# Kernel tuning notes

Hardware: AMD Instinct MI355X
Metric: run time of the kernel (lower is better)

Reference implementation:

```python
import jax, jax.numpy as jnp
import numpy as np
from jax import lax

BN_EPS = 1e-5


def binarize(v):
    """Sign binarization with clipped straight-through estimator.
    Forward: sign(v). Backward: grad * 1{|v| <= 1} (hardtanh STE), matching
    the standard 1w1a BinaryFunction used in XNOR/IR-Net style repos."""
    clipped = jnp.clip(v, -1.0, 1.0)
    return clipped + lax.stop_gradient(jnp.sign(v) - clipped)


def setup_inputs() -> dict:
    key = jax.random.key(0)
    k1, k2, k3, k4 = jax.random.split(key, 4)
    x = jax.random.normal(k1, (32, 256, 56, 56), dtype=jnp.float32)
    w = jax.random.normal(k2, (256, 256, 3, 3), dtype=jnp.float32) * 0.05
    gamma = jax.random.uniform(k3, (256,), dtype=jnp.float32, minval=0.5, maxval=1.5)
    beta = jax.random.normal(k4, (256,), dtype=jnp.float32) * 0.1
    return {"x": x, "w": w, "gamma": gamma, "beta": beta}


def reference(x, w, gamma, beta):
    # Binarize activations and weights (1-bit each) -> XNOR-style conv in FP math.
    bx = binarize(x)                       # [N, C_in, H, W] in {-1, 0, +1}
    bw = binarize(w)                       # [C_out, C_in, kH, kW]
    y = lax.conv_general_dilated(
        bx, bw,
        window_strides=(1, 1),
        padding=((1, 1), (1, 1)),
        dimension_numbers=("NCHW", "OIHW", "NCHW"),
    )                                      # [N, C_out, H, W]
    # BatchNorm2d in training mode: batch statistics over N, H, W per channel.
    mean = jnp.mean(y, axis=(0, 2, 3))
    var = jnp.var(y, axis=(0, 2, 3))
    inv = lax.rsqrt(var + BN_EPS)
    out = (y - mean[None, :, None, None]) * (gamma * inv)[None, :, None, None] \
        + beta[None, :, None, None]
    return out
```

## Files before the change

kernel.cpp:

```cpp
#include <hip/hip_runtime.h>
#include <stdint.h>

typedef unsigned long long u64;
typedef unsigned int u32;
typedef int v4i  __attribute__((ext_vector_type(4)));
typedef int v16i __attribute__((ext_vector_type(16)));

#define N_IMG 32
#define C_IN  256
#define C_OUT 256
#define H     56
#define W     56
#define HW    (H*W)
#define NHW   (N_IMG*HW)
#define CHW   (C_IN*HW)

#define PX_BYTES  3211264
#define WPK_BYTES 589824
#define Y_OFF     (PX_BYTES + WPK_BYTES)

__global__ __launch_bounds__(256)
void pack_x_kernel(const float* __restrict__ x, u64* __restrict__ px) {
    int t = blockIdx.x * 256 + threadIdx.x;
    int w4   = t % 14;
    int r    = t / 14;
    int word = r & 3;
    int r2   = r >> 2;
    int h    = r2 % H;
    int n    = r2 / H;
    const float4* src = (const float4*)(x + ((size_t)(n*C_IN + word*64) * HW + h*W + w4*4));
    u64 b0 = 0, b1 = 0, b2 = 0, b3 = 0;
    #pragma unroll 8
    for (int j = 0; j < 64; ++j) {
        float4 v = src[(size_t)j * (HW/4)];
        b0 |= (u64)(__float_as_uint(v.x) >> 31) << j;
        b1 |= (u64)(__float_as_uint(v.y) >> 31) << j;
        b2 |= (u64)(__float_as_uint(v.z) >> 31) << j;
        b3 |= (u64)(__float_as_uint(v.w) >> 31) << j;
    }
    u64* dst = px + (((size_t)((n*H + h)*W + w4*4)) << 2) + word;
    dst[0] = b0; dst[4] = b1; dst[8] = b2; dst[12] = b3;
}

__global__ __launch_bounds__(256)
void pack_wpk_kernel(const float* __restrict__ wt, char* __restrict__ wpk) {
    int t = blockIdx.x * 256 + threadIdx.x;
    int co = t & 255;
    int tk = t >> 8;
    int tap = tk >> 3;
    int kb  = tk & 7;
    u32* out = (u32*)wpk + t*8;
    #pragma unroll
    for (int g = 0; g < 8; ++g) {
        u32 dw = 0;
        #pragma unroll
        for (int b = 0; b < 4; ++b) {
            int ci = kb*32 + 4*g + b;
            float v = wt[((size_t)(co*C_IN + ci)) * 9 + tap];
            u32 byte = (__float_as_uint(v) >> 31) ? 0xFFu : 0x01u;
            dw |= byte << (8*b);
        }
        out[g] = dw;
    }
}

__global__ __launch_bounds__(256, 2)
void conv_mfma_kernel(const u64* __restrict__ px, const char* __restrict__ wpk,
                      short* __restrict__ y) {
    __shared__ char lds[4*4*66*16];
    int bx = blockIdx.x;
    int n  = bx / 28;
    int h0 = (bx % 28) * 2;
    int cobase = blockIdx.y * 128;
    int tid = threadIdx.x;

    int wid   = tid >> 6;
    int lane  = tid & 63;
    int l31   = lane & 31;
    int lhalf = lane >> 5;
    int coq   = wid & 1;
    int pxh   = wid >> 1;
    int cot   = cobase + coq*64;

    int pj0 = pxh*64 + l31;
    int pj1 = pj0 + 32;
    int r0 = (pj0 >= 56) ? 1 : 0;
    int w0 = pj0 - 56*r0;
    int r1 = (pj1 >= 56) ? 1 : 0;
    int w1 = pj1 - 56*r1; if (w1 > 55) w1 = 55;

    v16i acc00 = {0,0,0,0,0,0,0,0,0,0,0,0,0,0,0,0};
    v16i acc01 = acc00;
    v16i acc10 = acc00;
    v16i acc11 = acc00;

    const v4i* wq = (const v4i*)wpk;

    #pragma unroll 1
    for (int ciq = 0; ciq < 4; ++ciq) {
        if (ciq) __syncthreads();
        for (int i = tid; i < 4*66; i += 256) {
            int row = i / 66;
            int wp  = i % 66;
            int hh = h0 + row - 1;
            int ww = wp - 1;
            bool valid = ((unsigned)hh < (unsigned)H) && ((unsigned)ww < (unsigned)W);
            u64 wv = 0;
            if (valid)
                wv = px[(((size_t)((n*H + hh)*W + ww)) << 2) + ciq];
            u32 basev = valid ? 0x01010101u : 0u;
            #pragma unroll
            for (int kc = 0; kc < 4; ++kc) {
                u32 bits = (u32)(wv >> (kc*16)) & 0xFFFFu;
                v4i ov;
                #pragma unroll
                for (int d = 0; d < 4; ++d) {
                    u32 sel = (bits >> (4*d)) & 0xFu;
                    u32 sp  = (sel * 0x204081u) & 0x01010101u;
                    u32 m   = (sp << 8) - (sp << 1);
                    ov[d] = (int)(basev + m);
                }
                *(v4i*)(lds + ((kc*264 + i) << 4)) = ov;
            }
        }
        __syncthreads();

        #pragma unroll
        for (int tap = 0; tap < 9; ++tap) {
            const int dw = tap % 3;
            const int rr = tap / 3;
            int i0 = (((r0 + rr)*66) + (w0 + dw)) << 4;
            int i1 = (((r1 + rr)*66) + (w1 + dw)) << 4;
            #pragma unroll
            for (int kb = 0; kb < 2; ++kb) {
                int kbg = ciq*2 + kb;
                int widx = ((tap*8 + kbg)*256 + cot + l31) << 1;
                v4i av0 = wq[widx | lhalf];
                v4i av1 = wq[(widx + 64) | lhalf];
                int kc = kb*2 + lhalf;
                v4i b0 = *(const v4i*)(lds + kc*4224 + i0);
                v4i b1 = *(const v4i*)(lds + kc*4224 + i1);
                acc00 = __builtin_amdgcn_mfma_i32_32x32x32_i8(av0, b0, acc00, 0, 0, 0);
                acc01 = __builtin_amdgcn_mfma_i32_32x32x32_i8(av0, b1, acc01, 0, 0, 0);
                acc10 = __builtin_amdgcn_mfma_i32_32x32x32_i8(av1, b0, acc10, 0, 0, 0);
                acc11 = __builtin_amdgcn_mfma_i32_32x32x32_i8(av1, b1, acc11, 0, 0, 0);
            }
        }
    }

    size_t yb0 = (size_t)n*CHW + (size_t)(cot + (lhalf << 2))*HW;
    size_t yb1 = yb0 + (size_t)32*HW;
    int hr0 = h0 + r0, hr1 = h0 + r1;
    bool full1 = !(pxh == 1 && l31 >= 16);
    {
        size_t o = yb0 + (size_t)hr0*W + w0;
        #pragma unroll
        for (int rg = 0; rg < 16; ++rg)
            y[o + (size_t)((rg&3) + 8*(rg>>2))*HW] = (short)acc00[rg];
    }
    {
        size_t o = yb1 + (size_t)hr0*W + w0;
        #pragma unroll
        for (int rg = 0; rg < 16; ++rg)
            y[o + (size_t)((rg&3) + 8*(rg>>2))*HW] = (short)acc10[rg];
    }
    if (full1) {
        size_t o = yb0 + (size_t)hr1*W + w1;
        #pragma unroll
        for (int rg = 0; rg < 16; ++rg)
            y[o + (size_t)((rg&3) + 8*(rg>>2))*HW] = (short)acc01[rg];
        o = yb1 + (size_t)hr1*W + w1;
        #pragma unroll
        for (int rg = 0; rg < 16; ++rg)
            y[o + (size_t)((rg&3) + 8*(rg>>2))*HW] = (short)acc11[rg];
    }
}

__global__ __launch_bounds__(256)
void stats_kernel(const short* __restrict__ y, long long* __restrict__ partials) {
    int slab = blockIdx.x;
    const int4* ys = (const int4*)(y + (size_t)slab * HW);
    int s = 0, sq = 0;
    for (int i = threadIdx.x; i < HW/8; i += 256) {
        int4 v = ys[i];
        int vv[4] = {v.x, v.y, v.z, v.w};
        #pragma unroll
        for (int k = 0; k < 4; ++k) {
            int lo = (short)(vv[k] & 0xFFFF);
            int hi = (short)(vv[k] >> 16);
            s  += lo + hi;
            sq += lo*lo + hi*hi;
        }
    }
    __shared__ int       rs[256];
    __shared__ long long rq[256];
    rs[threadIdx.x] = s;
    rq[threadIdx.x] = sq;
    __syncthreads();
    for (int off = 128; off > 0; off >>= 1) {
        if (threadIdx.x < off) {
            rs[threadIdx.x] += rs[threadIdx.x + off];
            rq[threadIdx.x] += rq[threadIdx.x + off];
        }
        __syncthreads();
    }
    if (threadIdx.x == 0) {
        partials[2*slab]   = rs[0];
        partials[2*slab+1] = rq[0];
    }
}

__global__ __launch_bounds__(256)
void apply_kernel(const short* __restrict__ y, const long long* __restrict__ partials,
                  const float* __restrict__ gamma, const float* __restrict__ beta,
                  float* __restrict__ out) {
    int slab = blockIdx.x;
    int co = slab & 255;
    long long S = 0, SS = 0;
    #pragma unroll 8
    for (int m = 0; m < N_IMG; ++m) {
        S  += partials[2*((m<<8) | co)];
        SS += partials[2*((m<<8) | co) + 1];
    }
    double mean = (double)S  * (1.0 / (double)NHW);
    double var  = (double)SS * (1.0 / (double)NHW) - mean*mean;
    float a = gamma[co] * rsqrtf((float)var + 1e-5f);
    float b = beta[co] - (float)mean * a;

    const int4* ys = (const int4*)(y + (size_t)slab * HW);
    float4*     os = (float4*)(out + (size_t)slab * HW);
    for (int i = threadIdx.x; i < HW/8; i += 256) {
        int4 v = ys[i];
        float4 f0, f1;
        f0.x = a * (float)((short)(v.x & 0xFFFF)) + b;
        f0.y = a * (float)((short)(v.x >> 16))    + b;
        f0.z = a * (float)((short)(v.y & 0xFFFF)) + b;
        f0.w = a * (float)((short)(v.y >> 16))    + b;
        f1.x = a * (float)((short)(v.z & 0xFFFF)) + b;
        f1.y = a * (float)((short)(v.z >> 16))    + b;
        f1.z = a * (float)((short)(v.w & 0xFFFF)) + b;
        f1.w = a * (float)((short)(v.w >> 16))    + b;
        os[2*i]   = f0;
        os[2*i+1] = f1;
    }
}

extern "C" void kernel_launch(void* const* d_in, const int* in_sizes, int n_in,
                              void* d_out, int out_size, void* d_ws, size_t ws_size,
                              hipStream_t stream) {
    const float* x     = (const float*)d_in[0];
    const float* wt    = (const float*)d_in[1];
    const float* gamma = (const float*)d_in[2];
    const float* beta  = (const float*)d_in[3];
    float* out = (float*)d_out;

    char* ws = (char*)d_ws;
    u64*   px  = (u64*)ws;
    char*  wpk = ws + PX_BYTES;
    short* y   = (short*)(ws + Y_OFF);
    long long* partials = (long long*)ws;

    hipLaunchKernelGGL(pack_x_kernel,   dim3(100352/256), dim3(256), 0, stream, x, px);
    hipLaunchKernelGGL(pack_wpk_kernel, dim3(72),         dim3(256), 0, stream, wt, wpk);
    hipLaunchKernelGGL(conv_mfma_kernel,dim3(896, 2),     dim3(256), 0, stream, px, wpk, y);
    hipLaunchKernelGGL(stats_kernel,    dim3(8192),       dim3(256), 0, stream, y, partials);
    hipLaunchKernelGGL(apply_kernel,    dim3(8192),       dim3(256), 0, stream, y, partials, gamma, beta, out);
}
```

Measured before the change: 285.9 us.

## Double-buffer LDS activation tiles and prefetch next channel quarter during MFMA

The conv kernel now keeps two LDS buffers for the expanded int8 activation tile. The global load for the next channel quarter is issued before the MFMA loop, and its expansion is written into the other buffer afterwards, so only one barrier is needed per iteration. Per-thread tile addresses and validity masks are precomputed once, replacing per-iteration index math and branches. LDS use doubles, about 33 KB per block, which may limit occupancy, and register pressure rises from holding the prefetched values.

```diff
diff --git a/kernel.cpp b/kernel.cpp
--- a/kernel.cpp
+++ b/kernel.cpp
@@ -64,15 +64,50 @@
     }
 }
 
+#define QBYTES 16896
+
 __global__ __launch_bounds__(256, 2)
 void conv_mfma_kernel(const u64* __restrict__ px, const char* __restrict__ wpk,
                       short* __restrict__ y) {
-    __shared__ char lds[4*4*66*16];
+    __shared__ char lds[2*QBYTES];
     int bx = blockIdx.x;
     int n  = bx / 28;
     int h0 = (bx % 28) * 2;
     int cobase = blockIdx.y * 128;
     int tid = threadIdx.x;
+
+    int rowA = tid / 66,        wpA = tid % 66;
+    int hhA = h0 + rowA - 1,    wwA = wpA - 1;
+    bool vA = ((unsigned)hhA < (unsigned)H) && ((unsigned)wwA < (unsigned)W);
+    size_t offA = vA ? (((size_t)((n*H + hhA)*W + wwA)) << 2) : 0;
+    u64 mA = vA ? ~0ull : 0ull;
+    u32 baseA = vA ? 0x01010101u : 0u;
+
+    int itB  = 256 + tid;
+    bool hasB = (tid < 8);
+    int rowB = itB / 66,        wpB = itB % 66;
+    int hhB = h0 + rowB - 1,    wwB = wpB - 1;
+    bool vB = hasB && ((unsigned)hhB < (unsigned)H) && ((unsigned)wwB < (unsigned)W);
+    size_t offB = vB ? (((size_t)((n*H + hhB)*W + wwB)) << 2) : 0;
+    u64 mB = vB ? ~0ull : 0ull;
+    u32 baseB = vB ? 0x01010101u : 0u;
+
+#define EXPAND_WRITE(BUF, IT, WV, BASE)                                     \
+    {                                                                       \
+        _Pragma("unroll")                                                   \
+        for (int kc = 0; kc < 4; ++kc) {                                    \
+            u32 bits = (u32)((WV) >> (kc*16)) & 0xFFFFu;                    \
+            v4i ov;                                                         \
+            _Pragma("unroll")                                               \
+            for (int d = 0; d < 4; ++d) {                                   \
+                u32 sel = (bits >> (4*d)) & 0xFu;                           \
+                u32 sp  = (sel * 0x204081u) & 0x01010101u;                  \
+                u32 m2  = (sp << 8) - (sp << 1);                            \
+                ov[d] = (int)((BASE) + m2);                                 \
+            }                                                               \
+            *(v4i*)((BUF) + ((kc*264 + (IT)) << 4)) = ov;                   \
+        }                                                                   \
+    }
 
     int wid   = tid >> 6;
     int lane  = tid & 63;
@@ -96,35 +131,25 @@
 
     const v4i* wq = (const v4i*)wpk;
 
+    {
+        u64 wv0 = px[offA + 0] & mA;
+        EXPAND_WRITE(lds, tid, wv0, baseA);
+        if (hasB) {
+            u64 wv0b = px[offB + 0] & mB;
+            EXPAND_WRITE(lds, itB, wv0b, baseB);
+        }
+    }
+    __syncthreads();
+
     #pragma unroll 1
     for (int ciq = 0; ciq < 4; ++ciq) {
-        if (ciq) __syncthreads();
-        for (int i = tid; i < 4*66; i += 256) {
-            int row = i / 66;
-            int wp  = i % 66;
-            int hh = h0 + row - 1;
-            int ww = wp - 1;
-            bool valid = ((unsigned)hh < (unsigned)H) && ((unsigned)ww < (unsigned)W);
-            u64 wv = 0;
-            if (valid)
-                wv = px[(((size_t)((n*H + hh)*W + ww)) << 2) + ciq];
-            u32 basev = valid ? 0x01010101u : 0u;
-            #pragma unroll
-            for (int kc = 0; kc < 4; ++kc) {
-                u32 bits = (u32)(wv >> (kc*16)) & 0xFFFFu;
-                v4i ov;
-                #pragma unroll
-                for (int d = 0; d < 4; ++d) {
-                    u32 sel = (bits >> (4*d)) & 0xFu;
-                    u32 sp  = (sel * 0x204081u) & 0x01010101u;
-                    u32 m   = (sp << 8) - (sp << 1);
-                    ov[d] = (int)(basev + m);
-                }
-                *(v4i*)(lds + ((kc*264 + i) << 4)) = ov;
-            }
-        }
-        __syncthreads();
-
+        u64 nA = 0, nB = 0;
+        if (ciq < 3) {
+            nA = px[offA + ciq + 1] & mA;
+            if (hasB) nB = px[offB + ciq + 1] & mB;
+        }
+
+        const char* buf = lds + (ciq & 1) * QBYTES;
         #pragma unroll
         for (int tap = 0; tap < 9; ++tap) {
             const int dw = tap % 3;
@@ -138,15 +163,23 @@
                 v4i av0 = wq[widx | lhalf];
                 v4i av1 = wq[(widx + 64) | lhalf];
                 int kc = kb*2 + lhalf;
-                v4i b0 = *(const v4i*)(lds + kc*4224 + i0);
-                v4i b1 = *(const v4i*)(lds + kc*4224 + i1);
+                v4i b0 = *(const v4i*)(buf + kc*4224 + i0);
+                v4i b1 = *(const v4i*)(buf + kc*4224 + i1);
                 acc00 = __builtin_amdgcn_mfma_i32_32x32x32_i8(av0, b0, acc00, 0, 0, 0);
                 acc01 = __builtin_amdgcn_mfma_i32_32x32x32_i8(av0, b1, acc01, 0, 0, 0);
                 acc10 = __builtin_amdgcn_mfma_i32_32x32x32_i8(av1, b0, acc10, 0, 0, 0);
                 acc11 = __builtin_amdgcn_mfma_i32_32x32x32_i8(av1, b1, acc11, 0, 0, 0);
             }
         }
-    }
+
+        if (ciq < 3) {
+            char* nbuf = lds + ((ciq + 1) & 1) * QBYTES;
+            EXPAND_WRITE(nbuf, tid, nA, baseA);
+            if (hasB) EXPAND_WRITE(nbuf, itB, nB, baseB);
+            __syncthreads();
+        }
+    }
+#undef EXPAND_WRITE
 
     size_t yb0 = (size_t)n*CHW + (size_t)(cot + (lhalf << 2))*HW;
     size_t yb1 = yb0 + (size_t)32*HW;
```

After: 291.9 us. 2.1% more time.
